# Kernel tuning notes

Measured on AMD Instinct MI355X. Metric: run time of the kernel, lower is better.

The kernel has to match this reference:

```python
import jax, jax.numpy as jnp
import numpy as np

N = 10000          # num_nodes
E_DIR = 160000     # directed random edges before symmetrization
B = 8              # batch
IN = 64            # input_size per node
UNITS = 64         # num_units
K = 2              # max_diffusion_step -> num_matrices = K + 1
LAMBDA_MAX = 1.5   # stand-in for eigsh largest-eigenvalue estimate


def _build_scaled_laplacian():
    # L_scaled = (2/lambda_max) * (I - D^-1/2 A D^-1/2) - I, as sparse COO
    rng = np.random.default_rng(0)
    src = rng.integers(0, N, E_DIR)
    dst = rng.integers(0, N, E_DIR)
    # symmetrize A = max(A, A^T) by duplicating edges both ways
    r = np.concatenate([src, dst])
    c = np.concatenate([dst, src])
    w = np.ones(2 * E_DIR, np.float32)
    deg = np.zeros(N, np.float32)
    np.add.at(deg, r, w)
    d_inv_sqrt = np.where(deg > 0, deg ** -0.5, 0.0).astype(np.float32)
    coef = np.float32(2.0 / LAMBDA_MAX)
    off_vals = (-coef * d_inv_sqrt[r] * d_inv_sqrt[c] * w).astype(np.float32)
    diag_idx = np.arange(N, dtype=np.int32)
    diag_vals = np.full(N, coef - 1.0, np.float32)
    rows = np.concatenate([r.astype(np.int32), diag_idx])
    cols = np.concatenate([c.astype(np.int32), diag_idx])
    vals = np.concatenate([off_vals, diag_vals])
    return rows, cols, vals  # nnz = 2*E_DIR + N = 330000


def setup_inputs() -> dict:
    key = jax.random.key(0)
    k_in, k_w = jax.random.split(key)
    rows, cols, vals = _build_scaled_laplacian()
    num_matrices = K + 1
    fan_in = IN * num_matrices
    xavier = np.sqrt(6.0 / (fan_in + UNITS)).astype(np.float32)
    return {
        "inputs": jax.random.normal(k_in, (B, N * IN), dtype=jnp.float32),
        "rows": jnp.asarray(rows),
        "cols": jnp.asarray(cols),
        "vals": jnp.asarray(vals),
        "weights": jax.random.uniform(k_w, (fan_in, UNITS), dtype=jnp.float32,
                                      minval=-xavier, maxval=xavier),
        "biases": jnp.zeros((UNITS,), dtype=jnp.float32),
    }


def reference(inputs, rows, cols, vals, weights, biases):
    batch = inputs.shape[0]
    x = inputs.reshape(batch, N, -1)              # [B, N, in]
    in_size = x.shape[2]
    # x0: [N, in*B]
    x0 = jnp.transpose(x, (1, 2, 0)).reshape(N, in_size * batch)

    def spmm(h):  # sparse Laplacian @ dense
        return jax.ops.segment_sum(vals[:, None] * h[cols], rows, num_segments=N)

    # Chebyshev recursion: T0 = x0, T1 = L x0, Tk = 2 L Tk-1 - Tk-2
    xs = [x0]
    x1 = spmm(x0)
    xs.append(x1)
    xk_1, xk_2 = x1, x0
    for _ in range(2, K + 1):
        x2 = 2.0 * spmm(xk_1) - xk_2
        xs.append(x2)
        xk_1, xk_2 = x2, xk_1

    num_matrices = K + 1
    xcat = jnp.stack(xs, axis=0)                              # [M, N, in*B]
    xcat = xcat.reshape(num_matrices, N, in_size, batch)      # [M, N, in, B]
    xcat = jnp.transpose(xcat, (3, 1, 2, 0))                  # [B, N, in, M]
    xcat = xcat.reshape(batch * N, in_size * num_matrices)
    out = xcat @ weights + biases
    return out.reshape(batch, N, UNITS)
```

## Files before the change

kernel.cpp:

```cpp
#include <hip/hip_runtime.h>
#include <hip/hip_fp16.h>

#define N_NODES 10000
#define BATCH   8
#define IN_SZ   64
#define UNITS   64
#define ROW_U   256
#define RCAP    96
#define STR     (N_NODES * 64)

typedef unsigned int uint;
typedef unsigned short ushort;
typedef __attribute__((ext_vector_type(8))) _Float16 half8;
typedef __attribute__((ext_vector_type(4))) float float4v;
typedef __attribute__((ext_vector_type(2))) uint uint2v;

__device__ inline uint f2bf_bits(float f) {
    uint u = __float_as_uint(f);
    uint r = ((u >> 16) & 1u) + 0x7FFFu;
    return (u + r) >> 16;
}
__device__ inline uint pack2h(float a, float b) {
    return (uint)__half_as_ushort(__float2half(a)) |
           ((uint)__half_as_ushort(__float2half(b)) << 16);
}
__device__ inline float h_lo(uint u) {
    return __half2float(__ushort_as_half((ushort)(u & 0xFFFFu)));
}
__device__ inline float h_hi(uint u) {
    return __half2float(__ushort_as_half((ushort)(u >> 16)));
}

__global__ __launch_bounds__(256) void k_transpose_scatter(
    const float4v* __restrict__ in4, uint* __restrict__ x0,
    const int* __restrict__ rows, const int* __restrict__ cols,
    const float* __restrict__ vals, int* __restrict__ cursor,
    uint* __restrict__ edges, int nnz) {
    int gid = blockIdx.x * 256 + threadIdx.x;
    if (gid < nnz) {
        int r   = rows[gid];
        int pos = r * RCAP + atomicAdd(&cursor[r], 1);
        edges[pos] = (uint)cols[gid] | (f2bf_bits(vals[gid]) << 16);
    }
    int i4 = gid & 15;
    int b  = (gid >> 4) & 7;
    int n  = gid >> 7;
    float4v v = __builtin_nontemporal_load(
        &in4[((size_t)b * N_NODES + n) * 16 + i4]);
    int c_u = b * 32 + i4 * 2;
    int q   = c_u >> 6;
    uint2v pk;
    pk.x = pack2h(v.x, v.y);
    pk.y = pack2h(v.z, v.w);
    __builtin_nontemporal_store(pk,
        (uint2v*)(x0 + (size_t)q * STR + (size_t)n * 64 + (c_u & 63)));
}

#define LOADE(EP, OFF)                                                        \
    _Pragma("unroll") for (int j = 0; j < 8; ++j) EP[j] = edges[(OFF) + j];

#define GATHERX(XR, EP)                                                       \
    _Pragma("unroll") for (int j = 0; j < 8; ++j) {                           \
        uint c = EP[j] & 0x3FFFu;                                             \
        if (c > N_NODES - 1) c = N_NODES - 1;     \
        XR[j] = xq[c * 64u + lane];              \
    }

#define FMA8(EP, XR, G0)                                                      \
    _Pragma("unroll") for (int j = 0; j < 8; ++j) {                           \
        uint vb = ((G0) + j < cnt) ? (EP[j] & 0xFFFF0000u) : 0u;    \
        float vj = __uint_as_float(vb);                                       \
        a0 += vj * h_lo(XR[j]);                            \
        a1 += vj * h_hi(XR[j]);                            \
    }

__global__ __launch_bounds__(256) void k_spmm(const int* __restrict__ cursor,
                                              const uint* __restrict__ edges,
                                              const uint* __restrict__ xin,
                                              uint* __restrict__ xout,
                                              const uint* __restrict__ xsub,
                                              float scale) {
    int L    = blockIdx.x;
    int q    = (L & 7) >> 1;
    int rb   = ((L >> 3) << 1) | (L & 1);
    int wave = threadIdx.x >> 6;
    uint lane = threadIdx.x & 63;
    int row  = rb * 4 + wave;

    const uint* xq = xin + (size_t)q * STR;
    int base = row * RCAP;
    int cnt  = __builtin_amdgcn_readfirstlane(cursor[row]);
    int nblk = (cnt + 7) >> 3;

    uint sx = 0;
    if (xsub) sx = __builtin_nontemporal_load(
        &xsub[(size_t)q * STR + (size_t)row * 64 + lane]);

    float a0 = 0.f, a1 = 0.f;

    uint epA[8], epB[8];
    uint xA[8], xB[8];

    LOADE(epA, base);
    GATHERX(xA, epA);

    int k = 0;
    for (; k + 2 <= nblk; k += 2) {
        LOADE(epB, base + 8 * (k + 1));
        GATHERX(xB, epB);
        FMA8(epA, xA, 8 * k);
        if (k + 2 < nblk) {
            LOADE(epA, base + 8 * (k + 2));
            GATHERX(xA, epA);
        }
        FMA8(epB, xB, 8 * (k + 1));
    }
    if (k < nblk) FMA8(epA, xA, 8 * k);

    float o0 = scale * a0, o1 = scale * a1;
    if (xsub) {
        o0 -= h_lo(sx);
        o1 -= h_hi(sx);
    }
    __builtin_nontemporal_store(pack2h(o0, o1),
        &xout[(size_t)q * STR + (size_t)row * 64 + lane]);
}

__global__ __launch_bounds__(256) void k_combine(const uint* __restrict__ x0,
                                                 const uint* __restrict__ x1,
                                                 const uint* __restrict__ x2,
                                                 const float* __restrict__ W,
                                                 const float* __restrict__ bias,
                                                 float* __restrict__ out) {
    __shared__ ushort sWt[64][200];
    int t    = threadIdx.x;
    int wave = t >> 6, lane = t & 63;
    int mrow = lane & 15, quad = lane >> 4;
    int L    = blockIdx.x;
    int b    = L & 7;
    int n0   = (L >> 3) * 64 + wave * 16;

    const uint* xs[3] = {x0, x1, x2};
    int an = n0 + mrow;
    if (an > N_NODES - 1) an = N_NODES - 1;

    half8 af[6];
#pragma unroll
    for (int kb = 0; kb < 6; ++kb) {
        int mat = kb >> 1;
        int c_u = b * 32 + (kb & 1) * 16 + quad * 4;
        int q   = c_u >> 6;
        af[kb] = __builtin_nontemporal_load(
            (const half8*)(xs[mat] + (size_t)q * STR + (size_t)an * 64 +
                           (c_u & 63)));
    }

    for (int e = t; e < 192 * 64; e += 256) {
        int f = e >> 6;
        int u = e & 63;
        int i = f / 3;
        int m = f - 3 * i;
        sWt[u][m * 64 + i] = __half_as_ushort(__float2half(W[e]));
    }
    __syncthreads();

    float4v acc[4];
#pragma unroll
    for (int ut = 0; ut < 4; ++ut) acc[ut] = (float4v){0.f, 0.f, 0.f, 0.f};

#pragma unroll
    for (int kb = 0; kb < 6; ++kb)
#pragma unroll
        for (int ut = 0; ut < 4; ++ut)
            acc[ut] = __builtin_amdgcn_mfma_f32_16x16x32_f16(
                af[kb],
                *(const half8*)&sWt[ut * 16 + mrow][kb * 32 + quad * 8],
                acc[ut], 0, 0, 0);

#pragma unroll
    for (int ut = 0; ut < 4; ++ut) {
        float bv = bias[ut * 16 + mrow];
        int u = ut * 16 + mrow;
#pragma unroll
        for (int r = 0; r < 4; ++r) {
            int n = n0 + quad * 4 + r;
            if (n < N_NODES)
                __builtin_nontemporal_store(acc[ut][r] + bv,
                    &out[((size_t)b * N_NODES + n) * UNITS + u]);
        }
    }
}

extern "C" void kernel_launch(void* const* d_in, const int* in_sizes, int n_in,
                              void* d_out, int out_size, void* d_ws, size_t ws_size,
                              hipStream_t stream) {
    const float* inputs = (const float*)d_in[0];
    const int*   rows   = (const int*)d_in[1];
    const int*   cols   = (const int*)d_in[2];
    const float* vals   = (const float*)d_in[3];
    const float* W      = (const float*)d_in[4];
    const float* bias   = (const float*)d_in[5];
    float*       out    = (float*)d_out;
    int nnz = in_sizes[1];

    char* p = (char*)d_ws;
    auto alloc = [&](size_t bytes) {
        char* r = p;
        p += (bytes + 255) & ~(size_t)255;
        return r;
    };
    uint* x0     = (uint*)alloc(sizeof(uint) * (size_t)N_NODES * ROW_U);
    uint* x1     = (uint*)alloc(sizeof(uint) * (size_t)N_NODES * ROW_U);
    uint* x2     = (uint*)alloc(sizeof(uint) * (size_t)N_NODES * ROW_U);
    int*  cursor = (int*)alloc(sizeof(int) * N_NODES);
    uint* edges  = (uint*)alloc(sizeof(uint) * (size_t)N_NODES * RCAP);

    (void)hipMemsetAsync(cursor, 0, sizeof(int) * N_NODES, stream);
    k_transpose_scatter<<<N_NODES / 2, 256, 0, stream>>>(
        (const float4v*)inputs, x0, rows, cols, vals, cursor, edges, nnz);
    k_spmm<<<N_NODES, 256, 0, stream>>>(cursor, edges, x0, x1, nullptr, 1.0f);
    k_spmm<<<N_NODES, 256, 0, stream>>>(cursor, edges, x1, x2, x0, 2.0f);
    k_combine<<<157 * 8, 256, 0, stream>>>(x0, x1, x2, W, bias, out);
}
```

Before: 184.6 us.

## Fuse scatter, two SpMM passes and combine into one persistent kernel with grid barriers

Replaces the four separate kernel launches (scatter/transpose, two SpMM passes, combine GEMM) with a single persistent kernel of 1024 blocks. The phases are separated by software grid-wide barriers built on an atomic counter. Each phase's work is distributed in grid-stride loops. This removes launch gaps and inter-kernel drain. It relies on all 1024 blocks being co-resident to avoid deadlock, and it drops the nontemporal hints on the intermediate stores and loads.

```diff
diff --git a/kernel.cpp b/kernel.cpp
--- a/kernel.cpp
+++ b/kernel.cpp
@@ -3,11 +3,10 @@
 
 #define N_NODES 10000
 #define BATCH   8
-#define IN_SZ   64
-#define UNITS   64
-#define ROW_U   256
 #define RCAP    96
 #define STR     (N_NODES * 64)
+#define NBLK    1024
+#define NTHR    256
 
 typedef unsigned int uint;
 typedef unsigned short ushort;
@@ -31,162 +30,166 @@
     return __half2float(__ushort_as_half((ushort)(u >> 16)));
 }
 
-__global__ __launch_bounds__(256) void k_transpose_scatter(
-    const float4v* __restrict__ in4, uint* __restrict__ x0,
+__device__ __forceinline__ void grid_barrier(int* bar, int target) {
+    __syncthreads();
+    if (threadIdx.x == 0) {
+        __threadfence();
+        atomicAdd(bar, 1);
+        while (__hip_atomic_load(bar, __ATOMIC_RELAXED,
+                                 __HIP_MEMORY_SCOPE_AGENT) < target)
+            __builtin_amdgcn_s_sleep(2);
+        __threadfence();
+    }
+    __syncthreads();
+}
+
+#define LOADE(EP, OFF)                                                        \
+    _Pragma("unroll") for (int jj = 0; jj < 8; ++jj) EP[jj] = edges[(OFF) + jj];
+
+#define GATHERX(XR, EP)                                                       \
+    _Pragma("unroll") for (int jj = 0; jj < 8; ++jj) {                        \
+        uint c = EP[jj] & 0x3FFFu;                                            \
+        if (c > N_NODES - 1) c = N_NODES - 1;     \
+        XR[jj] = xq[c * 64u + lane];             \
+    }
+
+#define FMA8(EP, XR, G0)                                                      \
+    _Pragma("unroll") for (int jj = 0; jj < 8; ++jj) {                        \
+        uint vb = ((G0) + jj < cnt) ? (EP[jj] & 0xFFFF0000u) : 0u;  \
+        float vj = __uint_as_float(vb);                                       \
+        a0 += vj * h_lo(XR[jj]);                           \
+        a1 += vj * h_hi(XR[jj]);                           \
+    }
+
+__device__ __forceinline__ void spmm_phase(
+    const int* __restrict__ cursor, const uint* __restrict__ edges,
+    const uint* __restrict__ xin, uint* __restrict__ xout,
+    const uint* __restrict__ xsub, float scale,
+    int B, int wave, uint lane)
+{
+    int q = (B & 7) >> 1;
+    const uint* xq = xin + (size_t)q * STR;
+    for (int j = (B >> 3); j < 1250; j += 128) {
+        int row  = (2 * j + (B & 1)) * 4 + wave;
+        int base = __builtin_amdgcn_readfirstlane(row * RCAP);
+        int cnt  = __builtin_amdgcn_readfirstlane(cursor[row]);
+        int nblk = (cnt + 7) >> 3;
+
+        uint sx = 0;
+        if (xsub) sx = xsub[(size_t)q * STR + (size_t)row * 64 + lane];
+
+        float a0 = 0.f, a1 = 0.f;
+        uint epA[8], epB[8], xA[8], xB[8];
+        LOADE(epA, base);
+        GATHERX(xA, epA);
+        int k = 0;
+        for (; k + 2 <= nblk; k += 2) {
+            LOADE(epB, base + 8 * (k + 1));
+            GATHERX(xB, epB);
+            FMA8(epA, xA, 8 * k);
+            if (k + 2 < nblk) {
+                LOADE(epA, base + 8 * (k + 2));
+                GATHERX(xA, epA);
+            }
+            FMA8(epB, xB, 8 * (k + 1));
+        }
+        if (k < nblk) FMA8(epA, xA, 8 * k);
+
+        float o0 = scale * a0, o1 = scale * a1;
+        if (xsub) { o0 -= h_lo(sx); o1 -= h_hi(sx); }
+        xout[(size_t)q * STR + (size_t)row * 64 + lane] = pack2h(o0, o1);
+    }
+}
+
+__global__ __launch_bounds__(NTHR, 4) void k_fused(
+    const float4v* __restrict__ in4,
     const int* __restrict__ rows, const int* __restrict__ cols,
-    const float* __restrict__ vals, int* __restrict__ cursor,
-    uint* __restrict__ edges, int nnz) {
-    int gid = blockIdx.x * 256 + threadIdx.x;
-    if (gid < nnz) {
-        int r   = rows[gid];
-        int pos = r * RCAP + atomicAdd(&cursor[r], 1);
-        edges[pos] = (uint)cols[gid] | (f2bf_bits(vals[gid]) << 16);
-    }
-    int i4 = gid & 15;
-    int b  = (gid >> 4) & 7;
-    int n  = gid >> 7;
-    float4v v = __builtin_nontemporal_load(
-        &in4[((size_t)b * N_NODES + n) * 16 + i4]);
-    int c_u = b * 32 + i4 * 2;
-    int q   = c_u >> 6;
-    uint2v pk;
-    pk.x = pack2h(v.x, v.y);
-    pk.y = pack2h(v.z, v.w);
-    __builtin_nontemporal_store(pk,
-        (uint2v*)(x0 + (size_t)q * STR + (size_t)n * 64 + (c_u & 63)));
-}
-
-#define LOADE(EP, OFF)                                                        \
-    _Pragma("unroll") for (int j = 0; j < 8; ++j) EP[j] = edges[(OFF) + j];
-
-#define GATHERX(XR, EP)                                                       \
-    _Pragma("unroll") for (int j = 0; j < 8; ++j) {                           \
-        uint c = EP[j] & 0x3FFFu;                                             \
-        if (c > N_NODES - 1) c = N_NODES - 1;     \
-        XR[j] = xq[c * 64u + lane];              \
-    }
-
-#define FMA8(EP, XR, G0)                                                      \
-    _Pragma("unroll") for (int j = 0; j < 8; ++j) {                           \
-        uint vb = ((G0) + j < cnt) ? (EP[j] & 0xFFFF0000u) : 0u;    \
-        float vj = __uint_as_float(vb);                                       \
-        a0 += vj * h_lo(XR[j]);                            \
-        a1 += vj * h_hi(XR[j]);                            \
-    }
-
-__global__ __launch_bounds__(256) void k_spmm(const int* __restrict__ cursor,
-                                              const uint* __restrict__ edges,
-                                              const uint* __restrict__ xin,
-                                              uint* __restrict__ xout,
-                                              const uint* __restrict__ xsub,
-                                              float scale) {
-    int L    = blockIdx.x;
-    int q    = (L & 7) >> 1;
-    int rb   = ((L >> 3) << 1) | (L & 1);
-    int wave = threadIdx.x >> 6;
-    uint lane = threadIdx.x & 63;
-    int row  = rb * 4 + wave;
-
-    const uint* xq = xin + (size_t)q * STR;
-    int base = row * RCAP;
-    int cnt  = __builtin_amdgcn_readfirstlane(cursor[row]);
-    int nblk = (cnt + 7) >> 3;
-
-    uint sx = 0;
-    if (xsub) sx = __builtin_nontemporal_load(
-        &xsub[(size_t)q * STR + (size_t)row * 64 + lane]);
-
-    float a0 = 0.f, a1 = 0.f;
-
-    uint epA[8], epB[8];
-    uint xA[8], xB[8];
-
-    LOADE(epA, base);
-    GATHERX(xA, epA);
-
-    int k = 0;
-    for (; k + 2 <= nblk; k += 2) {
-        LOADE(epB, base + 8 * (k + 1));
-        GATHERX(xB, epB);
-        FMA8(epA, xA, 8 * k);
-        if (k + 2 < nblk) {
-            LOADE(epA, base + 8 * (k + 2));
-            GATHERX(xA, epA);
-        }
-        FMA8(epB, xB, 8 * (k + 1));
-    }
-    if (k < nblk) FMA8(epA, xA, 8 * k);
-
-    float o0 = scale * a0, o1 = scale * a1;
-    if (xsub) {
-        o0 -= h_lo(sx);
-        o1 -= h_hi(sx);
-    }
-    __builtin_nontemporal_store(pack2h(o0, o1),
-        &xout[(size_t)q * STR + (size_t)row * 64 + lane]);
-}
-
-__global__ __launch_bounds__(256) void k_combine(const uint* __restrict__ x0,
-                                                 const uint* __restrict__ x1,
-                                                 const uint* __restrict__ x2,
-                                                 const float* __restrict__ W,
-                                                 const float* __restrict__ bias,
-                                                 float* __restrict__ out) {
+    const float* __restrict__ vals,
+    const float* __restrict__ W, const float* __restrict__ bias,
+    uint* __restrict__ x0, uint* __restrict__ x1, uint* __restrict__ x2,
+    int* __restrict__ cursor, uint* __restrict__ edges,
+    int* __restrict__ bar, float* __restrict__ out, int nnz)
+{
     __shared__ ushort sWt[64][200];
-    int t    = threadIdx.x;
-    int wave = t >> 6, lane = t & 63;
+    const int B    = blockIdx.x;
+    const int t    = threadIdx.x;
+    const int wave = t >> 6;
+    const uint lane = t & 63;
+
+    for (int gid = B * NTHR + t; gid < N_NODES * 128; gid += NBLK * NTHR) {
+        if (gid < nnz) {
+            int r   = rows[gid];
+            int pos = r * RCAP + atomicAdd(&cursor[r], 1);
+            edges[pos] = (uint)cols[gid] | (f2bf_bits(vals[gid]) << 16);
+        }
+        int i4 = gid & 15;
+        int b  = (gid >> 4) & 7;
+        int n  = gid >> 7;
+        float4v v = __builtin_nontemporal_load(
+            &in4[((size_t)b * N_NODES + n) * 16 + i4]);
+        int c_u = b * 32 + i4 * 2;
+        int q   = c_u >> 6;
+        uint2v pk;
+        pk.x = pack2h(v.x, v.y);
+        pk.y = pack2h(v.z, v.w);
+        *(uint2v*)(x0 + (size_t)q * STR + (size_t)n * 64 + (c_u & 63)) = pk;
+    }
+    grid_barrier(bar, NBLK);
+
+    spmm_phase(cursor, edges, x0, x1, nullptr, 1.0f, B, wave, lane);
+    grid_barrier(bar, 2 * NBLK);
+
+    spmm_phase(cursor, edges, x1, x2, x0, 2.0f, B, wave, lane);
+    grid_barrier(bar, 3 * NBLK);
+
+    for (int e = t; e < 192 * 64; e += NTHR) {
+        int f = e >> 6, u = e & 63;
+        int i = f / 3, m = f - 3 * i;
+        sWt[u][m * 64 + i] = __half_as_ushort(__float2half(W[e]));
+    }
+    __syncthreads();
+
     int mrow = lane & 15, quad = lane >> 4;
-    int L    = blockIdx.x;
-    int b    = L & 7;
-    int n0   = (L >> 3) * 64 + wave * 16;
-
+    int b = B & 7;
     const uint* xs[3] = {x0, x1, x2};
-    int an = n0 + mrow;
-    if (an > N_NODES - 1) an = N_NODES - 1;
-
-    half8 af[6];
-#pragma unroll
-    for (int kb = 0; kb < 6; ++kb) {
-        int mat = kb >> 1;
-        int c_u = b * 32 + (kb & 1) * 16 + quad * 4;
-        int q   = c_u >> 6;
-        af[kb] = __builtin_nontemporal_load(
-            (const half8*)(xs[mat] + (size_t)q * STR + (size_t)an * 64 +
-                           (c_u & 63)));
-    }
-
-    for (int e = t; e < 192 * 64; e += 256) {
-        int f = e >> 6;
-        int u = e & 63;
-        int i = f / 3;
-        int m = f - 3 * i;
-        sWt[u][m * 64 + i] = __half_as_ushort(__float2half(W[e]));
-    }
-    __syncthreads();
-
-    float4v acc[4];
-#pragma unroll
-    for (int ut = 0; ut < 4; ++ut) acc[ut] = (float4v){0.f, 0.f, 0.f, 0.f};
-
-#pragma unroll
-    for (int kb = 0; kb < 6; ++kb)
-#pragma unroll
-        for (int ut = 0; ut < 4; ++ut)
-            acc[ut] = __builtin_amdgcn_mfma_f32_16x16x32_f16(
-                af[kb],
-                *(const half8*)&sWt[ut * 16 + mrow][kb * 32 + quad * 8],
-                acc[ut], 0, 0, 0);
-
-#pragma unroll
-    for (int ut = 0; ut < 4; ++ut) {
-        float bv = bias[ut * 16 + mrow];
-        int u = ut * 16 + mrow;
-#pragma unroll
-        for (int r = 0; r < 4; ++r) {
-            int n = n0 + quad * 4 + r;
-            if (n < N_NODES)
-                __builtin_nontemporal_store(acc[ut][r] + bv,
-                    &out[((size_t)b * N_NODES + n) * UNITS + u]);
+    for (int m = (B >> 3); m < 157; m += 128) {
+        int n0 = m * 64 + wave * 16;
+        int an = n0 + mrow;
+        if (an > N_NODES - 1) an = N_NODES - 1;
+
+        half8 af[6];
+#pragma unroll
+        for (int kb = 0; kb < 6; ++kb) {
+            int mat = kb >> 1;
+            int c_u = b * 32 + (kb & 1) * 16 + quad * 4;
+            int q   = c_u >> 6;
+            af[kb] = *(const half8*)(xs[mat] + (size_t)q * STR +
+                                     (size_t)an * 64 + (c_u & 63));
+        }
+
+        float4v acc[4];
+#pragma unroll
+        for (int ut = 0; ut < 4; ++ut) acc[ut] = (float4v){0.f, 0.f, 0.f, 0.f};
+#pragma unroll
+        for (int kb = 0; kb < 6; ++kb)
+#pragma unroll
+            for (int ut = 0; ut < 4; ++ut)
+                acc[ut] = __builtin_amdgcn_mfma_f32_16x16x32_f16(
+                    af[kb],
+                    *(const half8*)&sWt[ut * 16 + mrow][kb * 32 + quad * 8],
+                    acc[ut], 0, 0, 0);
+
+#pragma unroll
+        for (int ut = 0; ut < 4; ++ut) {
+            float bv = bias[ut * 16 + mrow];
+            int u = ut * 16 + mrow;
+#pragma unroll
+            for (int r = 0; r < 4; ++r) {
+                int n = n0 + quad * 4 + r;
+                if (n < N_NODES)
+                    __builtin_nontemporal_store(acc[ut][r] + bv,
+                        &out[((size_t)b * N_NODES + n) * 64 + u]);
+            }
         }
     }
 }
@@ -209,16 +212,15 @@
         p += (bytes + 255) & ~(size_t)255;
         return r;
     };
-    uint* x0     = (uint*)alloc(sizeof(uint) * (size_t)N_NODES * ROW_U);
-    uint* x1     = (uint*)alloc(sizeof(uint) * (size_t)N_NODES * ROW_U);
-    uint* x2     = (uint*)alloc(sizeof(uint) * (size_t)N_NODES * ROW_U);
-    int*  cursor = (int*)alloc(sizeof(int) * N_NODES);
+    uint* x0     = (uint*)alloc(sizeof(uint) * (size_t)N_NODES * 256);
+    uint* x1     = (uint*)alloc(sizeof(uint) * (size_t)N_NODES * 256);
+    uint* x2     = (uint*)alloc(sizeof(uint) * (size_t)N_NODES * 256);
+    int*  cursor = (int*)alloc(sizeof(int) * (N_NODES + 64));
     uint* edges  = (uint*)alloc(sizeof(uint) * (size_t)N_NODES * RCAP);
-
-    (void)hipMemsetAsync(cursor, 0, sizeof(int) * N_NODES, stream);
-    k_transpose_scatter<<<N_NODES / 2, 256, 0, stream>>>(
-        (const float4v*)inputs, x0, rows, cols, vals, cursor, edges, nnz);
-    k_spmm<<<N_NODES, 256, 0, stream>>>(cursor, edges, x0, x1, nullptr, 1.0f);
-    k_spmm<<<N_NODES, 256, 0, stream>>>(cursor, edges, x1, x2, x0, 2.0f);
-    k_combine<<<157 * 8, 256, 0, stream>>>(x0, x1, x2, W, bias, out);
-}
+    int*  bar    = cursor + N_NODES;
+
+    (void)hipMemsetAsync(cursor, 0, sizeof(int) * (N_NODES + 64), stream);
+    k_fused<<<NBLK, NTHR, 0, stream>>>((const float4v*)inputs, rows, cols,
+                                       vals, W, bias, x0, x1, x2, cursor,
+                                       edges, bar, out, nnz);
+}
```

Result: slower. 597.3 us (+223.6%).
